# Performance work log

Measured on AMD Instinct MI355X. Metric: run time of the kernel, lower is better.

The kernel has to match this reference:

```python
import jax, jax.numpy as jnp
import numpy as np

BETA = 0.5
THR = 1.0
BN_EPS = 1e-5

@jax.custom_vjp
def spike(x):
    # heaviside fire: spk = 1[x > 0]
    return (x > 0).astype(x.dtype)

def _spike_fwd(x):
    return spike(x), x

def _spike_bwd(x, g):
    # snnTorch surrogate.atan(), alpha=2: grad = (alpha/2) / (1 + (pi/2*alpha*x)^2) = 1/(1+(pi*x)^2)
    return (g / (1.0 + (jnp.pi * x) ** 2),)

spike.defvjp(_spike_fwd, _spike_bwd)

def setup_inputs() -> dict:
    key = jax.random.key(0)
    ks = jax.random.split(key, 6)
    B, T, D, O = 512, 128, 512, 10
    data = jax.random.normal(ks[0], (B, T, D), dtype=jnp.float32)
    # deterministic Dropout(0.5) mask in {0, 2} (scaled by 1/keep_prob), time-major
    u = jax.random.uniform(ks[1], (T, B, D), dtype=jnp.float32)
    drop_mask = (u > 0.5).astype(jnp.float32) * 2.0
    W1 = jax.random.normal(ks[2], (D, D), dtype=jnp.float32) / np.sqrt(D)
    b1 = jax.random.normal(ks[3], (D,), dtype=jnp.float32) * 0.01
    gamma = jnp.ones((D,), dtype=jnp.float32)
    bn_beta = jnp.zeros((D,), dtype=jnp.float32)
    W2 = jax.random.normal(ks[4], (O, D), dtype=jnp.float32) / np.sqrt(D)
    b2 = jax.random.normal(ks[5], (O,), dtype=jnp.float32) * 0.01
    return {"data": data, "drop_mask": drop_mask, "W1": W1, "b1": b1,
            "gamma": gamma, "bn_beta": bn_beta, "W2": W2, "b2": b2}

def reference(data, drop_mask, W1, b1, gamma, bn_beta, W2, b2):
    B, T, D = data.shape
    O = W2.shape[0]
    xs = jnp.transpose(data, (1, 0, 2))  # [T, B, D] time-major

    def batchnorm(x):  # training-mode BatchNorm1d over batch dim
        mean = jnp.mean(x, axis=0)
        var = jnp.mean((x - mean) ** 2, axis=0)
        return gamma * (x - mean) * jax.lax.rsqrt(var + BN_EPS) + bn_beta

    def step(carry, inp):
        mem1, spk1, mem2, spk2 = carry
        xt, mt = inp
        cur1 = batchnorm((mt * xt) @ W1.T + b1)          # dropout -> linear -> BN
        mem1 = BETA * mem1 + cur1 - spk1 * THR           # Leaky, subtract reset
        spk1 = spike(mem1 - THR)
        cur2 = spk1 @ W2.T + b2
        mem2 = BETA * mem2 + cur2 - spk2 * THR
        spk2 = spike(mem2 - THR)
        return (mem1, spk1, mem2, spk2), spk2

    init = (jnp.zeros((B, D), data.dtype), jnp.zeros((B, D), data.dtype),
            jnp.zeros((B, O), data.dtype), jnp.zeros((B, O), data.dtype))
    _, spk_rec = jax.lax.scan(step, init, (xs, drop_mask))
    return spk_rec  # [T, B, out_size] == torch.stack(spk_rec)
```

## Files before the change

kernel.cpp:

```cpp
#include <hip/hip_runtime.h>
#include <math.h>

#define B_ 512
#define T_ 128
#define D_ 512
#define O_ 10

typedef unsigned int uint32;
typedef unsigned long long uint64;
typedef short bf16x8 __attribute__((ext_vector_type(8)));
typedef float f32x4 __attribute__((ext_vector_type(4)));

__device__ __forceinline__ uint32 bf16rne(float f) {
    uint32 u = __float_as_uint(f);
    return (u + 0x7FFFu + ((u >> 16) & 1u)) >> 16;
}
__device__ __forceinline__ float bf16f(uint32 h) { return __uint_as_float(h << 16); }

__global__ __launch_bounds__(256)
void presplitW_kernel(const float* __restrict__ W1, unsigned short* __restrict__ Wsp)
{
    const int idx = blockIdx.x * 256 + threadIdx.x;
    const float4 v = *(const float4*)(W1 + (size_t)idx * 4);
    float vv[4] = {v.x, v.y, v.z, v.w};
    uint32 c0[4], c1[4], c2[4];
#pragma unroll
    for (int i = 0; i < 4; ++i) {
        c0[i] = bf16rne(vv[i]);
        float r = vv[i] - bf16f(c0[i]);
        c1[i] = bf16rne(r);
        float r2 = r - bf16f(c1[i]);
        c2[i] = bf16rne(r2);
    }
    const size_t base = (size_t)idx * 4;
    uint2 w;
    w.x = c0[0] | (c0[1] << 16); w.y = c0[2] | (c0[3] << 16);
    *(uint2*)(Wsp + base) = w;
    w.x = c1[0] | (c1[1] << 16); w.y = c1[2] | (c1[3] << 16);
    *(uint2*)(Wsp + 262144 + base) = w;
    w.x = c2[0] | (c2[1] << 16); w.y = c2[2] | (c2[3] << 16);
    *(uint2*)(Wsp + 524288 + base) = w;
}

#define SPW 32
#define SPL (128*SPW)

__global__ __launch_bounds__(256)
void gemm1_kernel(const float* __restrict__ data, const float* __restrict__ drop,
                  const unsigned short* __restrict__ Wsp, const float* __restrict__ b1,
                  float* __restrict__ hbuf, double* __restrict__ pSum,
                  double* __restrict__ pSq, int t0, int Tc)
{
    __shared__ __align__(16) unsigned short As3[3 * SPL];
    __shared__ __align__(16) unsigned short Ws3[3 * SPL];

    const int tid = threadIdx.x;
    const int bid = blockIdx.x;
    const int xcd = bid & 7;
    const int rest = bid >> 3;
    const int yy = rest & 3;
    const int g = (rest >> 2) * 8 + xcd;

    const int R = g * 128;
    const int tc = R >> 9;
    const int b_base = R & 511;
    const int t = t0 + tc;
    const int d0 = yy * 128;

    const int w = tid >> 6;
    const int lane = tid & 63;
    const int wm = w & 1, wn = w >> 1;
    const int q = lane >> 4, r16 = lane & 15;

    f32x4 acc[4][4];
#pragma unroll
    for (int i = 0; i < 4; ++i)
#pragma unroll
        for (int j = 0; j < 4; ++j) acc[i][j] = (f32x4){0.f, 0.f, 0.f, 0.f};

    for (int k0 = 0; k0 < 512; k0 += 32) {
#pragma unroll
        for (int i = 0; i < 2; ++i) {
            const int p = tid + i * 256;
            const int m = p >> 2;
            const int qg = p & 3;
            const int kg = qg * 8;
            const float* dsrc = data + ((size_t)(b_base + m) * T_ + t) * D_ + k0 + kg;
            const float* msrc = drop + ((size_t)t * B_ + b_base + m) * D_ + k0 + kg;
            const float4 dv0 = *(const float4*)(dsrc);
            const float4 dv1 = *(const float4*)(dsrc + 4);
            const float4 mv0 = *(const float4*)(msrc);
            const float4 mv1 = *(const float4*)(msrc + 4);
            float vv[8] = {dv0.x*mv0.x, dv0.y*mv0.y, dv0.z*mv0.z, dv0.w*mv0.w,
                           dv1.x*mv1.x, dv1.y*mv1.y, dv1.z*mv1.z, dv1.w*mv1.w};
            uint32 u0[8], u1[8], u2[8];
#pragma unroll
            for (int e = 0; e < 8; ++e) {
                u0[e] = bf16rne(vv[e]);
                const float r = vv[e] - bf16f(u0[e]);
                u1[e] = bf16rne(r);
                const float r2 = r - bf16f(u1[e]);
                u2[e] = bf16rne(r2);
            }
            const int qs = qg ^ ((m >> 1) & 3);
            const int dst = m * SPW + qs * 8;
            uint4 pk;
            pk.x = u0[0]|(u0[1]<<16); pk.y = u0[2]|(u0[3]<<16);
            pk.z = u0[4]|(u0[5]<<16); pk.w = u0[6]|(u0[7]<<16);
            *(uint4*)(&As3[dst]) = pk;
            pk.x = u1[0]|(u1[1]<<16); pk.y = u1[2]|(u1[3]<<16);
            pk.z = u1[4]|(u1[5]<<16); pk.w = u1[6]|(u1[7]<<16);
            *(uint4*)(&As3[SPL + dst]) = pk;
            pk.x = u2[0]|(u2[1]<<16); pk.y = u2[2]|(u2[3]<<16);
            pk.z = u2[4]|(u2[5]<<16); pk.w = u2[6]|(u2[7]<<16);
            *(uint4*)(&As3[2*SPL + dst]) = pk;
        }
#pragma unroll
        for (int i = 0; i < 6; ++i) {
            const int p = tid + i * 256;
            const int s = p >> 9;
            const int rem = p & 511;
            const int n = rem >> 2;
            const int qg = rem & 3;
            const int kg = qg * 8;
            const uint4 pk = *(const uint4*)(Wsp + (size_t)s * 262144
                                             + (size_t)(d0 + n) * 512 + k0 + kg);
            const int qs = qg ^ ((n >> 1) & 3);
            *(uint4*)(&Ws3[s * SPL + n * SPW + qs * 8]) = pk;
        }
        __syncthreads();

        const int qa = q ^ ((r16 >> 1) & 3);
        bf16x8 af[4][3], bfr[4][3];
#pragma unroll
        for (int mt = 0; mt < 4; ++mt)
#pragma unroll
            for (int s = 0; s < 3; ++s)
                af[mt][s] = *(const bf16x8*)(&As3[s*SPL + (wm*64 + mt*16 + r16)*SPW + qa*8]);
#pragma unroll
        for (int nt = 0; nt < 4; ++nt)
#pragma unroll
            for (int s = 0; s < 3; ++s)
                bfr[nt][s] = *(const bf16x8*)(&Ws3[s*SPL + (wn*64 + nt*16 + r16)*SPW + qa*8]);

#define PRODUCT(SA, SB)                                                          \
        {                                                                        \
            _Pragma("unroll")                                                    \
            for (int mt = 0; mt < 4; ++mt) {                                     \
                _Pragma("unroll")                                                \
                for (int nt = 0; nt < 4; ++nt)                                   \
                    acc[mt][nt] = __builtin_amdgcn_mfma_f32_16x16x32_bf16(       \
                        af[mt][SA], bfr[nt][SB], acc[mt][nt], 0, 0, 0);          \
            }                                                                    \
        }
        PRODUCT(0, 0)
        PRODUCT(0, 1)
        PRODUCT(1, 0)
        PRODUCT(1, 1)
        PRODUCT(0, 2)
        PRODUCT(2, 0)
#undef PRODUCT
        __syncthreads();
    }

    float b1c[4];
#pragma unroll
    for (int nt = 0; nt < 4; ++nt) b1c[nt] = b1[d0 + wn*64 + nt*16 + r16];

    double sd[4], sq[4];
#pragma unroll
    for (int nt = 0; nt < 4; ++nt) { sd[nt] = 0.0; sq[nt] = 0.0; }

#pragma unroll
    for (int mt = 0; mt < 4; ++mt)
#pragma unroll
        for (int r = 0; r < 4; ++r) {
            const int row = R + wm*64 + mt*16 + q*4 + r;
            float* op = hbuf + (size_t)row * D_ + d0 + wn*64 + r16;
#pragma unroll
            for (int nt = 0; nt < 4; ++nt) {
                const float hf = acc[mt][nt][r] + b1c[nt];
                op[nt*16] = hf;
                const double dh = (double)hf;
                sd[nt] += dh;
                sq[nt] = fma(dh, dh, sq[nt]);
            }
        }
#pragma unroll
    for (int nt = 0; nt < 4; ++nt) {
        sd[nt] += __shfl_xor(sd[nt], 16); sd[nt] += __shfl_xor(sd[nt], 32);
        sq[nt] += __shfl_xor(sq[nt], 16); sq[nt] += __shfl_xor(sq[nt], 32);
    }
    double* dsh = (double*)&As3[0];
    __syncthreads();
    if (q == 0) {
#pragma unroll
        for (int nt = 0; nt < 4; ++nt) {
            dsh[(w*64 + nt*16 + r16)*2 + 0] = sd[nt];
            dsh[(w*64 + nt*16 + r16)*2 + 1] = sq[nt];
        }
    }
    __syncthreads();
    if (tid < 128) {
        const int col = tid;
        const int gg = col >> 6, c = col & 63;
        const double S = dsh[((2*gg)*64 + c)*2 + 0] + dsh[((2*gg+1)*64 + c)*2 + 0];
        const double Q = dsh[((2*gg)*64 + c)*2 + 1] + dsh[((2*gg+1)*64 + c)*2 + 1];
        const int bt = b_base >> 7;
        pSum[((size_t)(bt*Tc + tc))*D_ + d0 + col] = S;
        pSq [((size_t)(bt*Tc + tc))*D_ + d0 + col] = Q;
    }
}

__global__ __launch_bounds__(256)
void finalize_kernel(const double* __restrict__ pSum, const double* __restrict__ pSq,
                     const float* __restrict__ gamma, const float* __restrict__ bn_beta,
                     float* __restrict__ scaleArr, float* __restrict__ shiftArr, int Tc)
{
    const int tc = blockIdx.x;
    const int d = blockIdx.y * 256 + threadIdx.x;
    double S = 0.0, Q = 0.0;
#pragma unroll
    for (int bt = 0; bt < 4; ++bt) {
        S += pSum[((size_t)(bt * Tc + tc)) * D_ + d];
        Q += pSq [((size_t)(bt * Tc + tc)) * D_ + d];
    }
    const double mean = S / (double)B_;
    const double var  = Q / (double)B_ - mean * mean;
    const double rs   = 1.0 / sqrt(var + 1e-5);
    const double gm   = (double)gamma[d] * rs;
    scaleArr[tc * D_ + d] = (float)gm;
    shiftArr[tc * D_ + d] = (float)((double)bn_beta[d] - gm * mean);
}

__global__ __launch_bounds__(256)
void scanA_kernel(const float* __restrict__ hbuf, const float* __restrict__ scaleArr,
                  const float* __restrict__ shiftArr, uint64* __restrict__ spkM,
                  float* __restrict__ sMem1, float* __restrict__ sSpk1, int t0, int Tc)
{
    const int e = blockIdx.x * 256 + threadIdx.x;
    const int d = e & 511;
    const int lane = threadIdx.x & 63;
    const int mword = (e >> 6);

    float m1, s1;
    if (t0 == 0) { m1 = 0.f; s1 = 0.f; }
    else { m1 = sMem1[e]; s1 = sSpk1[e]; }

    float hv[4], sc[4], sf[4];
#pragma unroll
    for (int j = 0; j < 4; ++j) {
        const int tcj = (j < Tc) ? j : (Tc - 1);
        hv[j] = hbuf[(size_t)tcj * (B_ * D_) + e];
        sc[j] = scaleArr[tcj * D_ + d];
        sf[j] = shiftArr[tcj * D_ + d];
    }

    for (int tc = 0; tc < Tc; tc += 4) {
        float hvN[4], scN[4], sfN[4];
#pragma unroll
        for (int j = 0; j < 4; ++j) {
            int tn = tc + 4 + j; tn = (tn < Tc) ? tn : (Tc - 1);
            hvN[j] = hbuf[(size_t)tn * (B_ * D_) + e];
            scN[j] = scaleArr[tn * D_ + d];
            sfN[j] = shiftArr[tn * D_ + d];
        }
#pragma unroll
        for (int j = 0; j < 4; ++j) {
            if (tc + j < Tc) {
                const float cur1 = fmaf(sc[j], hv[j], sf[j]);
                m1 = fmaf(0.5f, m1, cur1) - s1;
                s1 = ((m1 - 1.0f) > 0.f) ? 1.f : 0.f;
                const uint64 mask = __ballot(s1 == 1.f);
                if (lane == 0)
                    spkM[(size_t)(tc + j) * (B_ * 8) + mword] = mask;
            }
        }
#pragma unroll
        for (int j = 0; j < 4; ++j) { hv[j] = hvN[j]; sc[j] = scN[j]; sf[j] = sfN[j]; }
    }

    sMem1[e] = m1;
    sSpk1[e] = s1;
}

__global__ __launch_bounds__(256)
void gemm2_kernel(const uint64* __restrict__ spkM, const float* __restrict__ W2,
                  const float* __restrict__ b2, float* __restrict__ cur2)
{
    const int g = blockIdx.x * 256 + threadIdx.x;
    const int row = g >> 3;
    const int i = g & 7;
    const unsigned char* sp = (const unsigned char*)spkM;

    float P[8][O_];
#pragma unroll
    for (int c = 0; c < 8; ++c) {
        const uint32 byte = sp[(size_t)row * 64 + c * 8 + i];
        float f[8];
#pragma unroll
        for (int j = 0; j < 8; ++j)
            f[j] = (byte & (1u << j)) ? 1.0f : 0.0f;
#pragma unroll
        for (int o = 0; o < O_; ++o) {
            const float* wp = W2 + o * D_ + (i + 8 * c) * 8;
            const float4 wa = *(const float4*)(wp);
            const float4 wb = *(const float4*)(wp + 4);
            float v = f[0] * wa.x;
            v = fmaf(f[1], wa.y, v); v = fmaf(f[2], wa.z, v); v = fmaf(f[3], wa.w, v);
            v = fmaf(f[4], wb.x, v); v = fmaf(f[5], wb.y, v); v = fmaf(f[6], wb.z, v);
            v = fmaf(f[7], wb.w, v);
            P[c][o] = v;
        }
    }

    float p[O_];
#pragma unroll
    for (int o = 0; o < O_; ++o) {
        const float a1 = P[0][o] + P[4][o];
        const float a2 = P[2][o] + P[6][o];
        const float a3 = P[1][o] + P[5][o];
        const float a4 = P[3][o] + P[7][o];
        p[o] = (a1 + a2) + (a3 + a4);
    }
#pragma unroll
    for (int o = 0; o < O_; ++o) {
        p[o] += __shfl_xor(p[o], 4);
        p[o] += __shfl_xor(p[o], 2);
        p[o] += __shfl_xor(p[o], 1);
    }

    float out0 = 0.f, out1 = 0.f;
#pragma unroll
    for (int o = 0; o < 8; ++o)
        if (i == o) out0 = p[o] + b2[o];
    if (i == 0) out1 = p[8] + b2[8];
    if (i == 1) out1 = p[9] + b2[9];
    cur2[(size_t)row * O_ + i] = out0;
    if (i < 2)
        cur2[(size_t)row * O_ + 8 + i] = out1;
}

__global__ __launch_bounds__(256)
void scanB_kernel(const float* __restrict__ cur2, float* __restrict__ out,
                  float* __restrict__ sMem2, float* __restrict__ sSpk2, int t0, int Tc)
{
    const int idx = blockIdx.x * 256 + threadIdx.x;
    float mem2, spk2;
    if (t0 == 0) { mem2 = 0.f; spk2 = 0.f; }
    else { mem2 = sMem2[idx]; spk2 = sSpk2[idx]; }

    float v[4], vn[4];
#pragma unroll
    for (int j = 0; j < 4; ++j) v[j] = cur2[(size_t)j * (B_ * O_) + idx];

    for (int tg = 0; tg < Tc; tg += 4) {
        if (tg + 4 < Tc) {
#pragma unroll
            for (int j = 0; j < 4; ++j)
                vn[j] = cur2[(size_t)(tg + 4 + j) * (B_ * O_) + idx];
        }
#pragma unroll
        for (int j = 0; j < 4; ++j) {
            mem2 = fmaf(0.5f, mem2, v[j]) - spk2;
            spk2 = ((mem2 - 1.0f) > 0.f) ? 1.f : 0.f;
            out[(size_t)(t0 + tg + j) * (B_ * O_) + idx] = spk2;
        }
#pragma unroll
        for (int j = 0; j < 4; ++j) v[j] = vn[j];
    }
    sMem2[idx] = mem2;
    sSpk2[idx] = spk2;
}

extern "C" void kernel_launch(void* const* d_in, const int* in_sizes, int n_in,
                              void* d_out, int out_size, void* d_ws, size_t ws_size,
                              hipStream_t stream) {
    const float* data    = (const float*)d_in[0];
    const float* drop    = (const float*)d_in[1];
    const float* W1      = (const float*)d_in[2];
    const float* b1      = (const float*)d_in[3];
    const float* gamma   = (const float*)d_in[4];
    const float* bn_beta = (const float*)d_in[5];
    const float* W2      = (const float*)d_in[6];
    const float* b2      = (const float*)d_in[7];
    float* out = (float*)d_out;

    const size_t fixedBytes = 1572864 + 2*1048576 + 2*20480;
    const size_t perT = 1048576 + 32768 + 20480 + 4096 + 32768;
    int Tc = T_;
    while (Tc > 2 && fixedBytes + (size_t)Tc * perT > ws_size) Tc >>= 1;

    char* p = (char*)d_ws;
    double* pSum    = (double*)p; p += (size_t)4 * Tc * D_ * 8;
    double* pSq     = (double*)p; p += (size_t)4 * Tc * D_ * 8;
    float* hbuf     = (float*)p; p += (size_t)Tc * B_ * D_ * 4;
    float* scaleArr = (float*)p; p += (size_t)Tc * D_ * 4;
    float* shiftArr = (float*)p; p += (size_t)Tc * D_ * 4;
    float* sMem1    = (float*)p; p += (size_t)B_ * D_ * 4;
    float* sSpk1    = (float*)p; p += (size_t)B_ * D_ * 4;
    float* sMem2    = (float*)p; p += (size_t)B_ * O_ * 4;
    float* sSpk2    = (float*)p; p += (size_t)B_ * O_ * 4;
    float* cur2     = (float*)p; p += (size_t)Tc * B_ * O_ * 4;
    unsigned short* Wsp = (unsigned short*)p; p += (size_t)3 * D_ * D_ * 2;
    uint64* spkM    = (uint64*)p; p += (size_t)Tc * B_ * 8 * 8;

    presplitW_kernel<<<256, 256, 0, stream>>>(W1, Wsp);

    for (int t0 = 0; t0 < T_; t0 += Tc) {
        gemm1_kernel<<<Tc * 16, 256, 0, stream>>>(data, drop, Wsp, b1, hbuf,
                                                  pSum, pSq, t0, Tc);
        finalize_kernel<<<dim3(Tc, D_ / 256), 256, 0, stream>>>(
            pSum, pSq, gamma, bn_beta, scaleArr, shiftArr, Tc);
        scanA_kernel<<<(B_ * D_) / 256, 256, 0, stream>>>(hbuf, scaleArr, shiftArr, spkM,
                                                          sMem1, sSpk1, t0, Tc);
        gemm2_kernel<<<Tc * 16, 256, 0, stream>>>(spkM, W2, b2, cur2);
        scanB_kernel<<<20, 256, 0, stream>>>(cur2, out, sMem2, sSpk2, t0, Tc);
    }
}
```

Measured before the change: 510.9 us.

## Prefetch next A tile into registers and load W tiles directly to LDS

Loads of the next k-slice of data and dropout mask are issued into registers right after the current LDS fragments are read. This lets global-memory latency overlap with the MFMA work. The presplit W tiles are now copied with global_load_lds straight into LDS, with the swizzle moved to the source address, so they no longer pass through VGPRs. The three-way bf16 split is also packed two values at a time. The cost is higher register pressure and a dependence on the LDS layout matching the lane-contiguous order that global_load_lds writes.

```diff
diff --git a/kernel.cpp b/kernel.cpp
--- a/kernel.cpp
+++ b/kernel.cpp
@@ -16,6 +16,16 @@
     return (u + 0x7FFFu + ((u >> 16) & 1u)) >> 16;
 }
 __device__ __forceinline__ float bf16f(uint32 h) { return __uint_as_float(h << 16); }
+
+__device__ __forceinline__ uint32 pkbf16(float lo, float hi) {
+    return bf16rne(lo) | (bf16rne(hi) << 16);
+}
+
+__device__ __forceinline__ void gload16_lds(const void* g, void* l) {
+    __builtin_amdgcn_global_load_lds(
+        (const __attribute__((address_space(1))) unsigned int*)g,
+        (__attribute__((address_space(3))) unsigned int*)l, 16, 0, 0);
+}
 
 __global__ __launch_bounds__(256)
 void presplitW_kernel(const float* __restrict__ W1, unsigned short* __restrict__ Wsp)
@@ -78,55 +88,64 @@
 #pragma unroll
         for (int j = 0; j < 4; ++j) acc[i][j] = (f32x4){0.f, 0.f, 0.f, 0.f};
 
+    int dstA[2];
+    const float* dsrc[2];
+    const float* msrc[2];
+#pragma unroll
+    for (int i = 0; i < 2; ++i) {
+        const int p = tid + i * 256;
+        const int m = p >> 2;
+        const int qg = p & 3;
+        dstA[i] = m * SPW + (qg ^ ((m >> 1) & 3)) * 8;
+        dsrc[i] = data + ((size_t)(b_base + m) * T_ + t) * D_ + qg * 8;
+        msrc[i] = drop + ((size_t)t * B_ + b_base + m) * D_ + qg * 8;
+    }
+    float4 dR[2][2], mR[2][2];
+#pragma unroll
+    for (int i = 0; i < 2; ++i) {
+        dR[i][0] = *(const float4*)(dsrc[i]);
+        dR[i][1] = *(const float4*)(dsrc[i] + 4);
+        mR[i][0] = *(const float4*)(msrc[i]);
+        mR[i][1] = *(const float4*)(msrc[i] + 4);
+    }
+
     for (int k0 = 0; k0 < 512; k0 += 32) {
-#pragma unroll
-        for (int i = 0; i < 2; ++i) {
-            const int p = tid + i * 256;
-            const int m = p >> 2;
-            const int qg = p & 3;
-            const int kg = qg * 8;
-            const float* dsrc = data + ((size_t)(b_base + m) * T_ + t) * D_ + k0 + kg;
-            const float* msrc = drop + ((size_t)t * B_ + b_base + m) * D_ + k0 + kg;
-            const float4 dv0 = *(const float4*)(dsrc);
-            const float4 dv1 = *(const float4*)(dsrc + 4);
-            const float4 mv0 = *(const float4*)(msrc);
-            const float4 mv1 = *(const float4*)(msrc + 4);
-            float vv[8] = {dv0.x*mv0.x, dv0.y*mv0.y, dv0.z*mv0.z, dv0.w*mv0.w,
-                           dv1.x*mv1.x, dv1.y*mv1.y, dv1.z*mv1.z, dv1.w*mv1.w};
-            uint32 u0[8], u1[8], u2[8];
-#pragma unroll
-            for (int e = 0; e < 8; ++e) {
-                u0[e] = bf16rne(vv[e]);
-                const float r = vv[e] - bf16f(u0[e]);
-                u1[e] = bf16rne(r);
-                const float r2 = r - bf16f(u1[e]);
-                u2[e] = bf16rne(r2);
-            }
-            const int qs = qg ^ ((m >> 1) & 3);
-            const int dst = m * SPW + qs * 8;
-            uint4 pk;
-            pk.x = u0[0]|(u0[1]<<16); pk.y = u0[2]|(u0[3]<<16);
-            pk.z = u0[4]|(u0[5]<<16); pk.w = u0[6]|(u0[7]<<16);
-            *(uint4*)(&As3[dst]) = pk;
-            pk.x = u1[0]|(u1[1]<<16); pk.y = u1[2]|(u1[3]<<16);
-            pk.z = u1[4]|(u1[5]<<16); pk.w = u1[6]|(u1[7]<<16);
-            *(uint4*)(&As3[SPL + dst]) = pk;
-            pk.x = u2[0]|(u2[1]<<16); pk.y = u2[2]|(u2[3]<<16);
-            pk.z = u2[4]|(u2[5]<<16); pk.w = u2[6]|(u2[7]<<16);
-            *(uint4*)(&As3[2*SPL + dst]) = pk;
-        }
 #pragma unroll
         for (int i = 0; i < 6; ++i) {
             const int p = tid + i * 256;
             const int s = p >> 9;
             const int rem = p & 511;
             const int n = rem >> 2;
-            const int qg = rem & 3;
-            const int kg = qg * 8;
-            const uint4 pk = *(const uint4*)(Wsp + (size_t)s * 262144
-                                             + (size_t)(d0 + n) * 512 + k0 + kg);
-            const int qs = qg ^ ((n >> 1) & 3);
-            *(uint4*)(&Ws3[s * SPL + n * SPW + qs * 8]) = pk;
+            const int qs = rem & 3;
+            const int qg = qs ^ ((n >> 1) & 3);
+            gload16_lds(Wsp + (size_t)s * 262144 + (size_t)(d0 + n) * 512 + k0 + qg * 8,
+                        &Ws3[(size_t)p * 8]);
+        }
+#pragma unroll
+        for (int i = 0; i < 2; ++i) {
+            float vv[8] = {dR[i][0].x*mR[i][0].x, dR[i][0].y*mR[i][0].y,
+                           dR[i][0].z*mR[i][0].z, dR[i][0].w*mR[i][0].w,
+                           dR[i][1].x*mR[i][1].x, dR[i][1].y*mR[i][1].y,
+                           dR[i][1].z*mR[i][1].z, dR[i][1].w*mR[i][1].w};
+            uint32 q0[4], q1[4], q2[4];
+#pragma unroll
+            for (int pr = 0; pr < 4; ++pr) {
+                const float a = vv[2*pr], b = vv[2*pr+1];
+                q0[pr] = pkbf16(a, b);
+                const float ra = a - __uint_as_float(q0[pr] << 16);
+                const float rb = b - __uint_as_float(q0[pr] & 0xFFFF0000u);
+                q1[pr] = pkbf16(ra, rb);
+                const float sa = ra - __uint_as_float(q1[pr] << 16);
+                const float sb = rb - __uint_as_float(q1[pr] & 0xFFFF0000u);
+                q2[pr] = pkbf16(sa, sb);
+            }
+            uint4 pk;
+            pk.x = q0[0]; pk.y = q0[1]; pk.z = q0[2]; pk.w = q0[3];
+            *(uint4*)(&As3[dstA[i]]) = pk;
+            pk.x = q1[0]; pk.y = q1[1]; pk.z = q1[2]; pk.w = q1[3];
+            *(uint4*)(&As3[SPL + dstA[i]]) = pk;
+            pk.x = q2[0]; pk.y = q2[1]; pk.z = q2[2]; pk.w = q2[3];
+            *(uint4*)(&As3[2*SPL + dstA[i]]) = pk;
         }
         __syncthreads();
 
@@ -142,6 +161,17 @@
 #pragma unroll
             for (int s = 0; s < 3; ++s)
                 bfr[nt][s] = *(const bf16x8*)(&Ws3[s*SPL + (wn*64 + nt*16 + r16)*SPW + qa*8]);
+
+        if (k0 + 32 < 512) {
+            const int kn = k0 + 32;
+#pragma unroll
+            for (int i = 0; i < 2; ++i) {
+                dR[i][0] = *(const float4*)(dsrc[i] + kn);
+                dR[i][1] = *(const float4*)(dsrc[i] + kn + 4);
+                mR[i][0] = *(const float4*)(msrc[i] + kn);
+                mR[i][1] = *(const float4*)(msrc[i] + kn + 4);
+            }
+        }
 
 #define PRODUCT(SA, SB)                                                          \
         {                                                                        \
```

After: 510.3 us. About the same (-0.1%).
